# Performance work log

Hardware: AMD Instinct MI355X
Metric: run time of the kernel (lower is better)

## Reference

```python
import jax, jax.numpy as jnp
import numpy as np

CLASS_TOKEN_INDEX = 1
MAX_PROMPTS = 25
MAX_TEXT_LEN = 3500
THRESHOLD = 0.5
B, S, D, E = 8, 4096, 768, 128
P = E * (E - 1) // 2  # 8128 candidate span pairs


def setup_inputs() -> dict:
    rng = np.random.default_rng(0)
    input_ids = rng.integers(5, 30000, size=(B, S)).astype(np.int64)
    words_mask = np.zeros((B, S), dtype=np.int64)
    attention_mask = np.zeros((B, S), dtype=np.int64)
    text_lengths = np.zeros((B, 1), dtype=np.int64)
    for b in range(B):
        ns = int(rng.integers(10, MAX_PROMPTS + 1))  # number of entity-type prompt tokens
        input_ids[b][input_ids[b] == CLASS_TOKEN_INDEX] = 5  # remove stray specials
        input_ids[b, :ns] = CLASS_TOKEN_INDEX
        L = int(rng.integers(3000, MAX_TEXT_LEN + 1))  # number of words in text
        words_mask[b, ns:ns + L] = np.arange(1, L + 1)
        attention_mask[b, :ns + L] = 1
        text_lengths[b, 0] = L
    key = jax.random.key(0)
    k1, k2, k3 = jax.random.split(key, 3)
    return {
        "token_embeds": jax.random.normal(k1, (B, S, D), dtype=jnp.float32),
        "adj": jax.random.uniform(k2, (B, E, E), dtype=jnp.float32),
        "span_rep": jax.random.normal(k3, (B, E, D), dtype=jnp.float32),
        "input_ids": jnp.asarray(input_ids),
        "attention_mask": jnp.asarray(attention_mask),
        "text_lengths": jnp.asarray(text_lengths),
        "words_mask": jnp.asarray(words_mask),
    }


def _extract_special(token_embeds, input_ids):
    # pack embeddings at positions where input_ids == class token, left-aligned
    special = input_ids == CLASS_TOKEN_INDEX                      # (B,S)
    num_special = special.sum(-1, keepdims=True)                  # (B,1)
    slot = jnp.cumsum(special, axis=-1) - 1                       # packed slot per special
    tgt = jnp.where(special, slot, MAX_PROMPTS)                   # dump pads into extra slot
    bidx = jnp.arange(B)[:, None]
    emb = jnp.zeros((B, MAX_PROMPTS + 1, D), token_embeds.dtype)
    emb = emb.at[bidx, tgt].add(token_embeds * special[..., None].astype(token_embeds.dtype))
    emb = emb[:, :MAX_PROMPTS]
    mask = (jnp.arange(MAX_PROMPTS)[None, :] < num_special).astype(jnp.int64)
    return emb, mask


def _extract_words(token_embeds, words_mask, text_lengths):
    # scatter token embeddings into word slots: words_embedding[b, words_mask[b,j]-1] = token_embeds[b,j]
    is_word = words_mask > 0
    tgt = jnp.where(is_word, words_mask - 1, MAX_TEXT_LEN)        # dump pads into extra slot
    bidx = jnp.arange(B)[:, None]
    we = jnp.zeros((B, MAX_TEXT_LEN + 1, D), token_embeds.dtype)
    we = we.at[bidx, tgt].add(token_embeds * is_word[..., None].astype(token_embeds.dtype))
    we = we[:, :MAX_TEXT_LEN]
    mask = jnp.arange(MAX_TEXT_LEN)[None, :] < text_lengths       # (B,MAX_TEXT_LEN) bool
    return we, mask


def _build_entity_pairs(adj, span_rep):
    rows, cols = jnp.triu_indices(E, k=1)                         # (P,), (P,)
    vals = adj[:, rows, cols]                                     # (B,P)
    sel = vals > THRESHOLD
    # stable left-packing: selected pairs first, preserving triu order (matches per-batch torch loop)
    order = jnp.argsort((~sel).astype(jnp.int32), axis=1, stable=True)
    pair_mask = jnp.take_along_axis(sel, order, axis=1)           # (B,P) bool
    r = rows[order]                                               # (B,P)
    c = cols[order]
    pair_idx = jnp.where(pair_mask[..., None], jnp.stack([r, c], axis=-1), -1)
    bidx = jnp.arange(B)[:, None]
    head_rep = span_rep[bidx, jnp.where(pair_mask, r, 0)]         # pads gather span 0 (clamp_min(0))
    tail_rep = span_rep[bidx, jnp.where(pair_mask, c, 0)]
    return pair_idx, pair_mask, head_rep, tail_rep


def reference(token_embeds, adj, span_rep, input_ids, attention_mask, text_lengths, words_mask):
    prompts_embedding, prompts_embedding_mask = _extract_special(token_embeds, input_ids)
    words_embedding, word_mask = _extract_words(token_embeds, words_mask, text_lengths)
    pair_idx, pair_mask, head_rep, tail_rep = _build_entity_pairs(adj, span_rep)
    return (prompts_embedding, prompts_embedding_mask, words_embedding, word_mask,
            pair_idx, pair_mask, head_rep, tail_rep)
```

## Files before the change

### kernel.cpp

```cpp
#include <hip/hip_runtime.h>

#define BB 8
#define SS 4096
#define DD 768
#define EE 128
#define PP 8128
#define MP 25
#define MT 3500
#define D4 192
#define NROWS_W  (BB*MT)
#define NROWS_P  (BB*PP)
#define NROWS_PR (BB*MP)
#define R_TOTAL  (NROWS_W + 2*NROWS_P + NROWS_PR)

typedef float f32x4 __attribute__((ext_vector_type(4)));

__global__ __launch_bounds__(256) void k_prep(
    const int* __restrict__ ids, const float* __restrict__ adj,
    const int* __restrict__ wm, const int* __restrict__ tlen,
    float* __restrict__ out1, float* __restrict__ out3,
    float* __restrict__ out4, float* __restrict__ out5,
    int* __restrict__ wordpos, int* __restrict__ pairrec,
    int* __restrict__ pos)
{
    int blk = blockIdx.x;
    int role = blk >> 3, b = blk & 7;
    int t = threadIdx.x, wave = t >> 6, lane = t & 63;

    if (role == 0) {
        __shared__ int pos_s[32];
        __shared__ int spos[4 * 32];
        __shared__ int wcnt[4];
        __shared__ int woff[5];
        if (t < 32) pos_s[t] = -1;
        __syncthreads();
        const int* row = ids + b * SS;
        int base = 0;
        for (int c = 0; c < 16; ++c) {
            int p = wave * 1024 + c * 64 + lane;
            bool s = (row[p] == 1);
            unsigned long long m = __ballot(s);
            if (s) {
                int sl = base + __popcll(m & ((1ull << lane) - 1ull));
                if (sl < 32) spos[wave * 32 + sl] = p;
            }
            base += __popcll(m);
        }
        if (lane == 0) wcnt[wave] = base;
        __syncthreads();
        if (t == 0) {
            int acc = 0;
            for (int w = 0; w < 4; ++w) { woff[w] = acc; acc += wcnt[w]; }
            woff[4] = acc;
        }
        __syncthreads();
        {
            int cnt = wcnt[wave]; if (cnt > 32) cnt = 32;
            if (lane < cnt) {
                int g = woff[wave] + lane;
                if (g < MP) pos_s[g] = spos[wave * 32 + lane];
            }
        }
        __syncthreads();
        if (t < MP) {
            pos[b * MP + t] = pos_s[t];
            out1[b * MP + t] = (t < woff[4]) ? 1.0f : 0.0f;
        }
    } else if (role == 1) {
        int L = tlen[b];
        for (int i = t; i < MT; i += 256) {
            out3[b * MT + i] = (i < L) ? 1.0f : 0.0f;
            wordpos[b * MT + i] = -1;
        }
        __syncthreads();
        #pragma unroll 4
        for (int i = t; i < SS; i += 256) {
            int v = wm[b * SS + i];
            if (v > 0 && v <= MT) wordpos[b * MT + v - 1] = i;
        }
    } else {
        __shared__ int wsum[4];
        int p0 = t * 32;
        bool act = p0 < PP;
        int r0 = 0, c0 = 0;
        if (act) {
            int lo = 0, hi = EE - 2;
            while (lo < hi) {
                int mid = (lo + hi + 1) >> 1;
                int st = mid * (2 * EE - 1 - mid) / 2;
                if (st <= p0) lo = mid; else hi = mid - 1;
            }
            r0 = lo;
            c0 = r0 + 1 + (p0 - r0 * (2 * EE - 1 - r0) / 2);
        }
        unsigned selmask = 0;
        int my = 0;
        {
            int rr = r0, cc = c0;
            for (int i = 0; i < 32; ++i) {
                if (act && p0 + i < PP) {
                    bool s = adj[((size_t)b * EE + rr) * EE + cc] > 0.5f;
                    selmask |= (unsigned)s << i;
                    my += s ? 1 : 0;
                    if (++cc == EE) { ++rr; cc = rr + 1; }
                }
            }
        }
        int inc = my;
        for (int off = 1; off < 64; off <<= 1) {
            int n = __shfl_up(inc, off);
            if (lane >= off) inc += n;
        }
        if (lane == 63) wsum[wave] = inc;
        __syncthreads();
        int wv_off = 0, K = 0;
        for (int w = 0; w < 4; ++w) {
            int s = wsum[w];
            if (w < wave) wv_off += s;
            K += s;
        }
        int selb = wv_off + inc - my;
        {
            int rr = r0, cc = c0;
            for (int i = 0; i < 32; ++i) {
                int p = p0 + i;
                if (act && p < PP) {
                    bool s = (selmask >> i) & 1u;
                    int q;
                    if (s) { q = selb; ++selb; }
                    else   { q = K + (p - selb); }
                    size_t oq = (size_t)b * PP + q;
                    pairrec[oq] = s ? (int)(0x80000000u | ((unsigned)rr << 8) | (unsigned)cc) : 0;
                    out4[oq * 2 + 0] = s ? (float)rr : -1.0f;
                    out4[oq * 2 + 1] = s ? (float)cc : -1.0f;
                    out5[oq]         = s ? 1.0f : 0.0f;
                    if (++cc == EE) { ++rr; cc = rr + 1; }
                }
            }
        }
    }
}

__device__ __forceinline__ int row_index(const int* __restrict__ wordpos,
                                         const int* __restrict__ pairrec,
                                         const int* __restrict__ pos, int row) {
    if (row < NROWS_W) return wordpos[row];
    if (row < NROWS_W + 2 * NROWS_P) {
        int idx2 = row - NROWS_W;
        int idx = (idx2 < NROWS_P) ? idx2 : idx2 - NROWS_P;
        return pairrec[idx];
    }
    return pos[row - (NROWS_W + 2 * NROWS_P)];
}

__global__ __launch_bounds__(256) void k_gather(
    const float* __restrict__ te, const float* __restrict__ sr,
    const int* __restrict__ wordpos, const int* __restrict__ pairrec,
    const int* __restrict__ pos,
    float* __restrict__ out0, float* __restrict__ out2,
    float* __restrict__ out6, float* __restrict__ out7)
{
    int gw = blockIdx.x * 4 + (threadIdx.x >> 6);
    int lane = threadIdx.x & 63;
    int nw = gridDim.x * 4;
    const f32x4* te4 = (const f32x4*)te;
    const f32x4* sr4 = (const f32x4*)sr;

    int row = gw;
    int iv = (row < R_TOTAL) ? row_index(wordpos, pairrec, pos, row) : 0;
    for (; row < R_TOTAL; row += nw) {
        int cur = iv;
        int nrow = row + nw;
        if (nrow < R_TOTAL) iv = row_index(wordpos, pairrec, pos, nrow);

        const f32x4* src4;
        f32x4* dst4;
        bool valid = true;
        bool stream_src = false;
        if (row < NROWS_W) {
            int b = row / MT;
            valid = (cur >= 0);
            src4 = te4 + ((size_t)(b * SS + (valid ? cur : 0))) * D4;
            dst4 = (f32x4*)out2 + (size_t)row * D4;
            stream_src = true;
        } else if (row < NROWS_W + 2 * NROWS_P) {
            int idx2 = row - NROWS_W;
            bool head = idx2 < NROWS_P;
            int idx = head ? idx2 : idx2 - NROWS_P;
            int b = idx / PP;
            unsigned rec = (unsigned)cur;
            int s = head ? ((rec >> 8) & 0x7F) : (rec & 0xFF);
            src4 = sr4 + ((size_t)(b * EE + s)) * D4;
            dst4 = (f32x4*)(head ? out6 : out7) + (size_t)idx * D4;
        } else {
            int j2 = row - (NROWS_W + 2 * NROWS_P);
            int b = j2 / MP;
            valid = (cur >= 0);
            src4 = te4 + ((size_t)(b * SS + (valid ? cur : 0))) * D4;
            dst4 = (f32x4*)out0 + (size_t)j2 * D4;
            stream_src = true;
        }
        #pragma unroll
        for (int k = 0; k < 3; ++k) {
            f32x4 v = (f32x4)(0.0f);
            if (valid) {
                v = stream_src ? __builtin_nontemporal_load(&src4[lane + 64 * k])
                               : src4[lane + 64 * k];
            }
            dst4[lane + 64 * k] = v;
        }
    }
}

extern "C" void kernel_launch(void* const* d_in, const int* in_sizes, int n_in,
                              void* d_out, int out_size, void* d_ws, size_t ws_size,
                              hipStream_t stream) {
    const float* te   = (const float*)d_in[0];
    const float* adj  = (const float*)d_in[1];
    const float* sr   = (const float*)d_in[2];
    const int*   ids  = (const int*)d_in[3];
    const int*   tlen = (const int*)d_in[5];
    const int*   wm   = (const int*)d_in[6];
    float* out = (float*)d_out;

    size_t off0 = 0;
    size_t off1 = off0 + (size_t)BB * MP * DD;
    size_t off2 = off1 + (size_t)BB * MP;
    size_t off3 = off2 + (size_t)BB * MT * DD;
    size_t off4 = off3 + (size_t)BB * MT;
    size_t off5 = off4 + (size_t)BB * PP * 2;
    size_t off6 = off5 + (size_t)BB * PP;
    size_t off7 = off6 + (size_t)BB * PP * DD;

    int* wordpos = (int*)d_ws;
    int* pairrec = wordpos + BB * MT;
    int* pos     = pairrec + BB * PP;

    k_prep<<<24, 256, 0, stream>>>(ids, adj, wm, tlen,
                                   out + off1, out + off3, out + off4, out + off5,
                                   wordpos, pairrec, pos);
    k_gather<<<2048, 256, 0, stream>>>(te, sr, wordpos, pairrec, pos,
                                       out + off0, out + off2,
                                       out + off6, out + off7);
}
```

Measured before the change: 169.4 us.

## Fuse prep and gather into one cooperative kernel with grid sync

Merges the prep and gather kernels into a single cooperative launch of 1024 blocks. The 24 prep blocks do their work, then every block waits at a grid-wide barrier before the gather. The pair-selection prep now scans in 256-wide chunks with ballot and popcount, one pair per thread, instead of 32 serial pairs per thread. The gather drops the index-prefetch pipelining and uses half as many blocks. This removes one kernel launch gap, but most blocks sit idle at the barrier while the small prep runs, and the gather has fewer waves in flight.

```diff
diff --git a/kernel.cpp b/kernel.cpp
--- a/kernel.cpp
+++ b/kernel.cpp
@@ -1,4 +1,7 @@
 #include <hip/hip_runtime.h>
+#include <hip/hip_cooperative_groups.h>
+
+namespace cg = cooperative_groups;
 
 #define BB 8
 #define SS 4096
@@ -12,18 +15,38 @@
 #define NROWS_P  (BB*PP)
 #define NROWS_PR (BB*MP)
 #define R_TOTAL  (NROWS_W + 2*NROWS_P + NROWS_PR)
+#define GBLK 1024
+#define TBLK 256
 
 typedef float f32x4 __attribute__((ext_vector_type(4)));
 
-__global__ __launch_bounds__(256) void k_prep(
-    const int* __restrict__ ids, const float* __restrict__ adj,
-    const int* __restrict__ wm, const int* __restrict__ tlen,
-    float* __restrict__ out1, float* __restrict__ out3,
-    float* __restrict__ out4, float* __restrict__ out5,
-    int* __restrict__ wordpos, int* __restrict__ pairrec,
-    int* __restrict__ pos)
-{
-    int blk = blockIdx.x;
+#define OFF0 ((size_t)0)
+#define OFF1 (OFF0 + (size_t)BB*MP*DD)
+#define OFF2 (OFF1 + (size_t)BB*MP)
+#define OFF3 (OFF2 + (size_t)BB*MT*DD)
+#define OFF4 (OFF3 + (size_t)BB*MT)
+#define OFF5 (OFF4 + (size_t)BB*PP*2)
+#define OFF6 (OFF5 + (size_t)BB*PP)
+#define OFF7 (OFF6 + (size_t)BB*PP*DD)
+
+__device__ __forceinline__ int2 pair_rc(int p) {
+    int lo = 0, hi = EE - 2;
+    while (lo < hi) {
+        int mid = (lo + hi + 1) >> 1;
+        int st = mid * (2 * EE - 1 - mid) / 2;
+        if (st <= p) lo = mid; else hi = mid - 1;
+    }
+    int r = lo;
+    int c = r + 1 + (p - r * (2 * EE - 1 - r) / 2);
+    return make_int2(r, c);
+}
+
+__device__ void do_prep(int blk, const int* __restrict__ ids,
+                        const float* __restrict__ adj, const int* __restrict__ tlen,
+                        const int* __restrict__ wm, float* __restrict__ out,
+                        int* __restrict__ wordpos, int* __restrict__ pairrec,
+                        int* __restrict__ pos)
+{
     int role = blk >> 3, b = blk & 7;
     int t = threadIdx.x, wave = t >> 6, lane = t & 63;
 
@@ -64,140 +87,103 @@
         __syncthreads();
         if (t < MP) {
             pos[b * MP + t] = pos_s[t];
-            out1[b * MP + t] = (t < woff[4]) ? 1.0f : 0.0f;
+            out[OFF1 + b * MP + t] = (t < woff[4]) ? 1.0f : 0.0f;
         }
     } else if (role == 1) {
         int L = tlen[b];
-        for (int i = t; i < MT; i += 256) {
-            out3[b * MT + i] = (i < L) ? 1.0f : 0.0f;
+        for (int i = t; i < MT; i += TBLK) {
+            out[OFF3 + b * MT + i] = (i < L) ? 1.0f : 0.0f;
             wordpos[b * MT + i] = -1;
         }
         __syncthreads();
-        #pragma unroll 4
-        for (int i = t; i < SS; i += 256) {
+        for (int i = t; i < SS; i += TBLK) {
             int v = wm[b * SS + i];
             if (v > 0 && v <= MT) wordpos[b * MT + v - 1] = i;
         }
     } else {
-        __shared__ int wsum[4];
-        int p0 = t * 32;
-        bool act = p0 < PP;
-        int r0 = 0, c0 = 0;
-        if (act) {
-            int lo = 0, hi = EE - 2;
-            while (lo < hi) {
-                int mid = (lo + hi + 1) >> 1;
-                int st = mid * (2 * EE - 1 - mid) / 2;
-                if (st <= p0) lo = mid; else hi = mid - 1;
-            }
-            r0 = lo;
-            c0 = r0 + 1 + (p0 - r0 * (2 * EE - 1 - r0) / 2);
-        }
-        unsigned selmask = 0;
-        int my = 0;
-        {
-            int rr = r0, cc = c0;
-            for (int i = 0; i < 32; ++i) {
-                if (act && p0 + i < PP) {
-                    bool s = adj[((size_t)b * EE + rr) * EE + cc] > 0.5f;
-                    selmask |= (unsigned)s << i;
-                    my += s ? 1 : 0;
-                    if (++cc == EE) { ++rr; cc = rr + 1; }
+        __shared__ unsigned long long wmask[32][4];
+        __shared__ int wsum[32][4];
+        for (int ch = 0; ch < 32; ++ch) {
+            int p = ch * TBLK + t;
+            bool s = false;
+            if (p < PP) {
+                int2 rc = pair_rc(p);
+                s = adj[((size_t)b * EE + rc.x) * EE + rc.y] > 0.5f;
+            }
+            unsigned long long m = __ballot(s);
+            if (lane == 0) { wmask[ch][wave] = m; wsum[ch][wave] = __popcll(m); }
+        }
+        __syncthreads();
+        int K = 0;
+        for (int ch = 0; ch < 32; ++ch)
+            K += wsum[ch][0] + wsum[ch][1] + wsum[ch][2] + wsum[ch][3];
+        int cbase = 0;
+        for (int ch = 0; ch < 32; ++ch) {
+            int p = ch * TBLK + t;
+            if (p < PP) {
+                unsigned long long m = wmask[ch][wave];
+                bool s = (m >> lane) & 1ull;
+                int woffw = 0;
+                for (int w = 0; w < wave; ++w) woffw += wsum[ch][w];
+                int rank = cbase + woffw + __popcll(m & ((1ull << lane) - 1ull));
+                int q = s ? rank : (K + (p - rank));
+                size_t oq = (size_t)b * PP + q;
+                if (s) {
+                    int2 rc = pair_rc(p);
+                    pairrec[oq] = (int)(0x80000000u | ((unsigned)rc.x << 8) | (unsigned)rc.y);
+                    out[OFF4 + oq * 2 + 0] = (float)rc.x;
+                    out[OFF4 + oq * 2 + 1] = (float)rc.y;
+                    out[OFF5 + oq] = 1.0f;
+                } else {
+                    pairrec[oq] = 0;
+                    out[OFF4 + oq * 2 + 0] = -1.0f;
+                    out[OFF4 + oq * 2 + 1] = -1.0f;
+                    out[OFF5 + oq] = 0.0f;
                 }
             }
-        }
-        int inc = my;
-        for (int off = 1; off < 64; off <<= 1) {
-            int n = __shfl_up(inc, off);
-            if (lane >= off) inc += n;
-        }
-        if (lane == 63) wsum[wave] = inc;
-        __syncthreads();
-        int wv_off = 0, K = 0;
-        for (int w = 0; w < 4; ++w) {
-            int s = wsum[w];
-            if (w < wave) wv_off += s;
-            K += s;
-        }
-        int selb = wv_off + inc - my;
-        {
-            int rr = r0, cc = c0;
-            for (int i = 0; i < 32; ++i) {
-                int p = p0 + i;
-                if (act && p < PP) {
-                    bool s = (selmask >> i) & 1u;
-                    int q;
-                    if (s) { q = selb; ++selb; }
-                    else   { q = K + (p - selb); }
-                    size_t oq = (size_t)b * PP + q;
-                    pairrec[oq] = s ? (int)(0x80000000u | ((unsigned)rr << 8) | (unsigned)cc) : 0;
-                    out4[oq * 2 + 0] = s ? (float)rr : -1.0f;
-                    out4[oq * 2 + 1] = s ? (float)cc : -1.0f;
-                    out5[oq]         = s ? 1.0f : 0.0f;
-                    if (++cc == EE) { ++rr; cc = rr + 1; }
-                }
-            }
-        }
-    }
-}
-
-__device__ __forceinline__ int row_index(const int* __restrict__ wordpos,
-                                         const int* __restrict__ pairrec,
-                                         const int* __restrict__ pos, int row) {
-    if (row < NROWS_W) return wordpos[row];
-    if (row < NROWS_W + 2 * NROWS_P) {
-        int idx2 = row - NROWS_W;
-        int idx = (idx2 < NROWS_P) ? idx2 : idx2 - NROWS_P;
-        return pairrec[idx];
-    }
-    return pos[row - (NROWS_W + 2 * NROWS_P)];
-}
-
-__global__ __launch_bounds__(256) void k_gather(
-    const float* __restrict__ te, const float* __restrict__ sr,
-    const int* __restrict__ wordpos, const int* __restrict__ pairrec,
-    const int* __restrict__ pos,
-    float* __restrict__ out0, float* __restrict__ out2,
-    float* __restrict__ out6, float* __restrict__ out7)
-{
-    int gw = blockIdx.x * 4 + (threadIdx.x >> 6);
-    int lane = threadIdx.x & 63;
-    int nw = gridDim.x * 4;
+            cbase += wsum[ch][0] + wsum[ch][1] + wsum[ch][2] + wsum[ch][3];
+        }
+    }
+}
+
+__device__ void do_gather(int blk, int nblk,
+                          const float* __restrict__ te, const float* __restrict__ sr,
+                          const int* __restrict__ wordpos, const int* __restrict__ pairrec,
+                          const int* __restrict__ pos, float* __restrict__ out)
+{
+    int wave = threadIdx.x >> 6, lane = threadIdx.x & 63;
+    int gw = blk * (TBLK / 64) + wave;
+    int nw = nblk * (TBLK / 64);
     const f32x4* te4 = (const f32x4*)te;
     const f32x4* sr4 = (const f32x4*)sr;
-
-    int row = gw;
-    int iv = (row < R_TOTAL) ? row_index(wordpos, pairrec, pos, row) : 0;
-    for (; row < R_TOTAL; row += nw) {
-        int cur = iv;
-        int nrow = row + nw;
-        if (nrow < R_TOTAL) iv = row_index(wordpos, pairrec, pos, nrow);
-
+    for (int row = gw; row < R_TOTAL; row += nw) {
         const f32x4* src4;
         f32x4* dst4;
         bool valid = true;
         bool stream_src = false;
         if (row < NROWS_W) {
             int b = row / MT;
-            valid = (cur >= 0);
-            src4 = te4 + ((size_t)(b * SS + (valid ? cur : 0))) * D4;
-            dst4 = (f32x4*)out2 + (size_t)row * D4;
+            int s = wordpos[row];
+            valid = (s >= 0);
+            src4 = te4 + ((size_t)(b * SS + (valid ? s : 0))) * D4;
+            dst4 = (f32x4*)(out + OFF2) + (size_t)row * D4;
             stream_src = true;
         } else if (row < NROWS_W + 2 * NROWS_P) {
             int idx2 = row - NROWS_W;
             bool head = idx2 < NROWS_P;
             int idx = head ? idx2 : idx2 - NROWS_P;
             int b = idx / PP;
-            unsigned rec = (unsigned)cur;
+            unsigned rec = (unsigned)pairrec[idx];
             int s = head ? ((rec >> 8) & 0x7F) : (rec & 0xFF);
             src4 = sr4 + ((size_t)(b * EE + s)) * D4;
-            dst4 = (f32x4*)(head ? out6 : out7) + (size_t)idx * D4;
+            dst4 = (f32x4*)(out + (head ? OFF6 : OFF7)) + (size_t)idx * D4;
         } else {
             int j2 = row - (NROWS_W + 2 * NROWS_P);
             int b = j2 / MP;
-            valid = (cur >= 0);
-            src4 = te4 + ((size_t)(b * SS + (valid ? cur : 0))) * D4;
-            dst4 = (f32x4*)out0 + (size_t)j2 * D4;
+            int s = pos[j2];
+            valid = (s >= 0);
+            src4 = te4 + ((size_t)(b * SS + (valid ? s : 0))) * D4;
+            dst4 = (f32x4*)(out + OFF0) + (size_t)j2 * D4;
             stream_src = true;
         }
         #pragma unroll
@@ -210,6 +196,37 @@
             dst4[lane + 64 * k] = v;
         }
     }
+}
+
+__global__ __launch_bounds__(TBLK, 4) void k_coop(
+    const float* __restrict__ te, const float* __restrict__ adj,
+    const float* __restrict__ sr, const int* __restrict__ ids,
+    const int* __restrict__ tlen, const int* __restrict__ wm,
+    float* __restrict__ out, int* __restrict__ wordpos,
+    int* __restrict__ pairrec, int* __restrict__ pos)
+{
+    int blk = blockIdx.x;
+    if (blk < 24) do_prep(blk, ids, adj, tlen, wm, out, wordpos, pairrec, pos);
+    __threadfence();
+    cg::this_grid().sync();
+    do_gather(blk, gridDim.x, te, sr, wordpos, pairrec, pos, out);
+}
+
+__global__ __launch_bounds__(TBLK) void k_prep_fb(
+    const float* __restrict__ adj, const int* __restrict__ ids,
+    const int* __restrict__ tlen, const int* __restrict__ wm,
+    float* __restrict__ out, int* __restrict__ wordpos,
+    int* __restrict__ pairrec, int* __restrict__ pos)
+{
+    do_prep(blockIdx.x, ids, adj, tlen, wm, out, wordpos, pairrec, pos);
+}
+
+__global__ __launch_bounds__(TBLK) void k_gather_fb(
+    const float* __restrict__ te, const float* __restrict__ sr,
+    const int* __restrict__ wordpos, const int* __restrict__ pairrec,
+    const int* __restrict__ pos, float* __restrict__ out)
+{
+    do_gather(blockIdx.x, gridDim.x, te, sr, wordpos, pairrec, pos, out);
 }
 
 extern "C" void kernel_launch(void* const* d_in, const int* in_sizes, int n_in,
@@ -223,23 +240,18 @@
     const int*   wm   = (const int*)d_in[6];
     float* out = (float*)d_out;
 
-    size_t off0 = 0;
-    size_t off1 = off0 + (size_t)BB * MP * DD;
-    size_t off2 = off1 + (size_t)BB * MP;
-    size_t off3 = off2 + (size_t)BB * MT * DD;
-    size_t off4 = off3 + (size_t)BB * MT;
-    size_t off5 = off4 + (size_t)BB * PP * 2;
-    size_t off6 = off5 + (size_t)BB * PP;
-    size_t off7 = off6 + (size_t)BB * PP * DD;
-
     int* wordpos = (int*)d_ws;
     int* pairrec = wordpos + BB * MT;
     int* pos     = pairrec + BB * PP;
 
-    k_prep<<<24, 256, 0, stream>>>(ids, adj, wm, tlen,
-                                   out + off1, out + off3, out + off4, out + off5,
-                                   wordpos, pairrec, pos);
-    k_gather<<<2048, 256, 0, stream>>>(te, sr, wordpos, pairrec, pos,
-                                       out + off0, out + off2,
-                                       out + off6, out + off7);
-}
+    void* args[] = { (void*)&te, (void*)&adj, (void*)&sr, (void*)&ids,
+                     (void*)&tlen, (void*)&wm, (void*)&out,
+                     (void*)&wordpos, (void*)&pairrec, (void*)&pos };
+    hipError_t err = hipLaunchCooperativeKernel((void*)k_coop, dim3(GBLK), dim3(TBLK),
+                                                args, 0, stream);
+    if (err != hipSuccess) {
+        k_prep_fb<<<24, TBLK, 0, stream>>>(adj, ids, tlen, wm, out,
+                                           wordpos, pairrec, pos);
+        k_gather_fb<<<GBLK, TBLK, 0, stream>>>(te, sr, wordpos, pairrec, pos, out);
+    }
+}
```

Result: slower. 309.5 us (+82.7%).
